# Performance work log

Hardware: AMD Instinct MI355X
Metric: run time of the kernel (lower is better)

## Reference

```python
import jax, jax.numpy as jnp
import numpy as np

B, S, D = 4, 4096, 1024

def setup_inputs() -> dict:
    key = jax.random.key(0)
    k1, k2 = jax.random.split(key)
    x = jax.random.normal(k1, (B, S, D), dtype=jnp.float32)
    W_qkv = jax.random.normal(k2, (D, 3 * D), dtype=jnp.float32) * (D ** -0.5)
    b_qkv = jnp.zeros((3 * D,), dtype=jnp.float32)
    return {"x": x, "W_qkv": W_qkv, "b_qkv": b_qkv}

def reference(x, W_qkv, b_qkv):
    # qkv projection: [B,S,3D]
    qkv = jnp.einsum('bsd,de->bse', x, W_qkv) + b_qkv
    q, k, v = jnp.split(qkv, 3, axis=-1)  # each [B,S,D]
    scale = q.shape[-1] ** -0.5
    # full [B,S,S] score matrix, as in the original (non-fused) implementation
    scores = jnp.einsum('bqd,bkd->bqk', q, k) * scale
    attn = jax.nn.softmax(scores, axis=-1)
    out = jnp.einsum('bqk,bkd->bqd', attn, v)
    return out
```

## Files before the change

### kernel.cpp

```cpp
#include <hip/hip_runtime.h>
#include <math.h>

typedef unsigned short ushort_t;
typedef __attribute__((ext_vector_type(8))) short short8;
typedef __attribute__((ext_vector_type(4))) float floatx4;

__device__ inline ushort_t f2bf(float x) {
    union { float f; unsigned int u; } c; c.f = x;
    unsigned int r = (c.u + 0x7fffu + ((c.u >> 16) & 1u)) >> 16;
    return (ushort_t)r;
}

__device__ __forceinline__ void glds16(const ushort_t* g, ushort_t* l) {
    __builtin_amdgcn_global_load_lds(
        (const __attribute__((address_space(1))) unsigned int*)g,
        (__attribute__((address_space(3))) unsigned int*)l,
        16, 0, 0);
}

__device__ __forceinline__ unsigned swzo(unsigned off) {
    return off ^ ((off >> 3) & 0x70u);
}

__global__ __launch_bounds__(256)
void wt_kernel(const float* __restrict__ W, ushort_t* __restrict__ Wt)
{
    __shared__ float tile[64][65];
    const int k0 = blockIdx.x * 64;
    const int n0 = blockIdx.y * 64;
    const int tid = threadIdx.x;
    #pragma unroll
    for (int ii = 0; ii < 16; ++ii) {
        int idx = ii * 256 + tid;
        int r = idx >> 6, c = idx & 63;
        tile[r][c] = W[(size_t)(k0 + r) * 3072 + n0 + c];
    }
    __syncthreads();
    #pragma unroll
    for (int ii = 0; ii < 16; ++ii) {
        int idx = ii * 256 + tid;
        int r = idx >> 6, c = idx & 63;
        Wt[(size_t)(n0 + r) * 1024 + k0 + c] = f2bf(tile[c][r]);
    }
}

__global__ __launch_bounds__(256)
void xcvt(const float* __restrict__ x, ushort_t* __restrict__ xb)
{
    const int i = (blockIdx.x * 256 + threadIdx.x) * 8;
    float4 f0 = *(const float4*)(x + i);
    float4 f1 = *(const float4*)(x + i + 4);
    ushort_t tmp[8] __attribute__((aligned(16)));
    tmp[0]=f2bf(f0.x); tmp[1]=f2bf(f0.y); tmp[2]=f2bf(f0.z); tmp[3]=f2bf(f0.w);
    tmp[4]=f2bf(f1.x); tmp[5]=f2bf(f1.y); tmp[6]=f2bf(f1.z); tmp[7]=f2bf(f1.w);
    *(uint4*)(xb + i) = *(const uint4*)tmp;
}

__global__ __launch_bounds__(256)
void qkv_mfma(const float* __restrict__ x, const ushort_t* __restrict__ Wt,
              const float* __restrict__ bias,
              ushort_t* __restrict__ q, ushort_t* __restrict__ k,
              ushort_t* __restrict__ vt)
{
    __shared__ ushort_t As[128][72];
    __shared__ ushort_t Bs[128][72];
    const int tid = threadIdx.x;
    const int w = tid >> 6, lane = tid & 63;
    const int m = lane & 15, quad = lane >> 4;
    const int col0 = blockIdx.x * 128;
    const int r0   = blockIdx.y * 128;

    floatx4 o[2][8];
    #pragma unroll
    for (int rf = 0; rf < 2; ++rf)
        #pragma unroll
        for (int nf = 0; nf < 8; ++nf)
            o[rf][nf] = (floatx4){0.f, 0.f, 0.f, 0.f};

    for (int kc = 0; kc < 16; ++kc) {
        const int kdim = kc * 64;
        __syncthreads();
        #pragma unroll
        for (int ii = 0; ii < 4; ++ii) {
            int lin = ii * 256 + tid;
            int row = lin >> 3, seg = lin & 7;
            const float* src = x + (size_t)(r0 + row) * 1024 + kdim + seg * 8;
            float4 f0 = *(const float4*)src;
            float4 f1 = *(const float4*)(src + 4);
            ushort_t tmp[8] __attribute__((aligned(16)));
            tmp[0]=f2bf(f0.x); tmp[1]=f2bf(f0.y); tmp[2]=f2bf(f0.z); tmp[3]=f2bf(f0.w);
            tmp[4]=f2bf(f1.x); tmp[5]=f2bf(f1.y); tmp[6]=f2bf(f1.z); tmp[7]=f2bf(f1.w);
            *(uint4*)&As[row][seg * 8] = *(const uint4*)tmp;
        }
        #pragma unroll
        for (int ii = 0; ii < 4; ++ii) {
            int lin = ii * 256 + tid;
            int row = lin >> 3, seg = lin & 7;
            const ushort_t* src = Wt + (size_t)(col0 + row) * 1024 + kdim + seg * 8;
            *(uint4*)&Bs[row][seg * 8] = *(const uint4*)src;
        }
        __syncthreads();
        #pragma unroll
        for (int kk = 0; kk < 2; ++kk) {
            short8 af[2];
            #pragma unroll
            for (int rf = 0; rf < 2; ++rf)
                af[rf] = *(const short8*)&As[w * 32 + rf * 16 + m][kk * 32 + quad * 8];
            #pragma unroll
            for (int nf = 0; nf < 8; ++nf) {
                short8 bf = *(const short8*)&Bs[nf * 16 + m][kk * 32 + quad * 8];
                #pragma unroll
                for (int rf = 0; rf < 2; ++rf)
                    o[rf][nf] = __builtin_amdgcn_mfma_f32_16x16x32_bf16(af[rf], bf, o[rf][nf], 0, 0, 0);
            }
        }
    }

    const int which = col0 >> 10;
    const int dbase = col0 & 1023;
    float bias_v[8];
    #pragma unroll
    for (int nf = 0; nf < 8; ++nf) bias_v[nf] = bias[col0 + nf * 16 + m];

    #pragma unroll
    for (int rf = 0; rf < 2; ++rf) {
        #pragma unroll
        for (int e = 0; e < 4; ++e) {
            const int g = r0 + w * 32 + rf * 16 + quad * 4 + e;
            #pragma unroll
            for (int nf = 0; nf < 8; ++nf) {
                const int c = dbase + nf * 16 + m;
                float val = o[rf][nf][e] + bias_v[nf];
                if (which == 0) {
                    q[(size_t)g * 1024 + c] = f2bf(val * 0.03125f);
                } else if (which == 1) {
                    k[(size_t)g * 1024 + c] = f2bf(val);
                } else {
                    vt[(size_t)(g >> 12) * 4194304 + (size_t)c * 4096 + (g & 4095)] = f2bf(val);
                }
            }
        }
    }
}

__global__ __launch_bounds__(256)
void qkv_mfma2(const ushort_t* __restrict__ xb, const ushort_t* __restrict__ Wt,
               const float* __restrict__ bias,
               ushort_t* __restrict__ q, ushort_t* __restrict__ k,
               ushort_t* __restrict__ vt)
{
    __shared__ __align__(1024) ushort_t As[128][64];
    __shared__ __align__(1024) ushort_t Bs[128][64];
    const int tid = threadIdx.x;
    const int w = tid >> 6, lane = tid & 63;
    const int m = lane & 15, quad = lane >> 4;
    const int lx = lane ^ ((lane >> 3) & 7);
    const int sr = lx >> 3, sc = (lx & 7) * 8;
    const int col0 = blockIdx.x * 128;
    const int r0   = blockIdx.y * 128;

    floatx4 o[2][8];
    #pragma unroll
    for (int rf = 0; rf < 2; ++rf)
        #pragma unroll
        for (int nf = 0; nf < 8; ++nf)
            o[rf][nf] = (floatx4){0.f, 0.f, 0.f, 0.f};

    for (int kc = 0; kc < 16; ++kc) {
        const int kdim = kc * 64;
        __syncthreads();
        #pragma unroll
        for (int ii = 0; ii < 4; ++ii) {
            glds16(xb + (size_t)(r0 + w * 32 + ii * 8 + sr) * 1024 + kdim + sc,
                   &As[w * 32 + ii * 8][0]);
            glds16(Wt + (size_t)(col0 + w * 32 + ii * 8 + sr) * 1024 + kdim + sc,
                   &Bs[w * 32 + ii * 8][0]);
        }
        __syncthreads();
        #pragma unroll
        for (int kk = 0; kk < 2; ++kk) {
            short8 af[2];
            #pragma unroll
            for (int rf = 0; rf < 2; ++rf)
                af[rf] = *(const short8*)((const char*)As +
                          swzo((unsigned)((w * 32 + rf * 16 + m) * 128 + kk * 64 + quad * 16)));
            #pragma unroll
            for (int nf = 0; nf < 8; ++nf) {
                short8 bf = *(const short8*)((const char*)Bs +
                          swzo((unsigned)((nf * 16 + m) * 128 + kk * 64 + quad * 16)));
                #pragma unroll
                for (int rf = 0; rf < 2; ++rf)
                    o[rf][nf] = __builtin_amdgcn_mfma_f32_16x16x32_bf16(af[rf], bf, o[rf][nf], 0, 0, 0);
            }
        }
    }

    const int which = col0 >> 10;
    const int dbase = col0 & 1023;
    float bias_v[8];
    #pragma unroll
    for (int nf = 0; nf < 8; ++nf) bias_v[nf] = bias[col0 + nf * 16 + m];

    #pragma unroll
    for (int rf = 0; rf < 2; ++rf) {
        #pragma unroll
        for (int e = 0; e < 4; ++e) {
            const int g = r0 + w * 32 + rf * 16 + quad * 4 + e;
            #pragma unroll
            for (int nf = 0; nf < 8; ++nf) {
                const int c = dbase + nf * 16 + m;
                float val = o[rf][nf][e] + bias_v[nf];
                if (which == 0) {
                    q[(size_t)g * 1024 + c] = f2bf(val * 0.03125f);
                } else if (which == 1) {
                    k[(size_t)g * 1024 + c] = f2bf(val);
                } else {
                    vt[(size_t)(g >> 12) * 4194304 + (size_t)c * 4096 + (g & 4095)] = f2bf(val);
                }
            }
        }
    }
}

__global__ __launch_bounds__(512, 2)
void fused_attn(const ushort_t* __restrict__ q, const ushort_t* __restrict__ kb_,
                const ushort_t* __restrict__ vt, float* __restrict__ out)
{
    __shared__ __align__(1024) unsigned char lds[135168];
    ushort_t (*Qs)[128][32] = (ushort_t(*)[128][32])(lds);
    ushort_t (*Ks)[256][32] = (ushort_t(*)[256][32])(lds + 16384);
    ushort_t (*Pls)[264]    = (ushort_t(*)[264])(lds);
    ushort_t (*Vs)[512][32] = (ushort_t(*)[512][32])(lds + 67584);
    float    (*redL)[4]     = (float(*)[4])(lds + 133120);

    const int tid  = threadIdx.x;
    const int w    = tid >> 6, lane = tid & 63;
    const int m    = lane & 15, quad = lane >> 4;
    const int wr   = w & 1, wc = w >> 1;
    const int lx   = lane ^ ((lane >> 3) & 7);
    const int lr   = lx >> 2, lc = (lx & 3) * 8;
    const int n0x  = blockIdx.x * 512;
    const int r0   = blockIdx.y * 128;
    const int b    = blockIdx.z;
    const size_t qoff = (size_t)b * 4096 * 1024;
    const size_t voff = (size_t)b * 4194304;

    unsigned qof[4], kof[4], vof[8];
    #pragma unroll
    for (int i = 0; i < 4; ++i)
        qof[i] = swzo((unsigned)((wr * 64 + i * 16 + m) * 64 + quad * 16));
    #pragma unroll
    for (int j = 0; j < 4; ++j)
        kof[j] = swzo((unsigned)((wc * 64 + j * 16 + m) * 64 + quad * 16));
    #pragma unroll
    for (int j = 0; j < 8; ++j)
        vof[j] = swzo((unsigned)((wc * 128 + j * 16 + m) * 64 + quad * 16));

    floatx4 o[4][8];
    #pragma unroll
    for (int i = 0; i < 4; ++i)
        #pragma unroll
        for (int j = 0; j < 8; ++j)
            o[i][j] = (floatx4){0.f, 0.f, 0.f, 0.f};
    float lsum[4][4] = {};

    for (int kt = 0; kt < 16; ++kt) {
        const int kbase = kt * 256;

        floatx4 s[4][4];
        #pragma unroll
        for (int i = 0; i < 4; ++i)
            #pragma unroll
            for (int j = 0; j < 4; ++j)
                s[i][j] = (floatx4){0.f, 0.f, 0.f, 0.f};

        {
            glds16(q   + qoff + (size_t)(r0 + w * 16 + lr) * 1024 + lc,             &Qs[0][w * 16][0]);
            glds16(kb_ + qoff + (size_t)(kbase + w * 32 + lr) * 1024 + lc,          &Ks[0][w * 32][0]);
            glds16(kb_ + qoff + (size_t)(kbase + w * 32 + 16 + lr) * 1024 + lc,     &Ks[0][w * 32 + 16][0]);
        }
        __syncthreads();
        for (int kc = 0; kc < 32; ++kc) {
            const int p = kc & 1;
            if (kc < 31) {
                const int kd = (kc + 1) * 32;
                glds16(q   + qoff + (size_t)(r0 + w * 16 + lr) * 1024 + kd + lc,         &Qs[p ^ 1][w * 16][0]);
                glds16(kb_ + qoff + (size_t)(kbase + w * 32 + lr) * 1024 + kd + lc,      &Ks[p ^ 1][w * 32][0]);
                glds16(kb_ + qoff + (size_t)(kbase + w * 32 + 16 + lr) * 1024 + kd + lc, &Ks[p ^ 1][w * 32 + 16][0]);
            }
            short8 af[4], bf[4];
            #pragma unroll
            for (int i = 0; i < 4; ++i)
                af[i] = *(const short8*)((const char*)Qs[p] + qof[i]);
            #pragma unroll
            for (int j = 0; j < 4; ++j)
                bf[j] = *(const short8*)((const char*)Ks[p] + kof[j]);
            #pragma unroll
            for (int i = 0; i < 4; ++i)
                #pragma unroll
                for (int j = 0; j < 4; ++j)
                    s[i][j] = __builtin_amdgcn_mfma_f32_16x16x32_bf16(af[i], bf[j], s[i][j], 0, 0, 0);
            __syncthreads();
        }

        #pragma unroll
        for (int i = 0; i < 4; ++i)
            #pragma unroll
            for (int j = 0; j < 4; ++j)
                #pragma unroll
                for (int e = 0; e < 4; ++e) {
                    float pv = __expf(s[i][j][e]);
                    lsum[i][e] += pv;
                    Pls[wr * 64 + i * 16 + quad * 4 + e][wc * 64 + j * 16 + m] = f2bf(pv);
                }

        {
            #pragma unroll
            for (int i = 0; i < 4; ++i)
                glds16(vt + voff + (size_t)(n0x + w * 64 + i * 16 + lr) * 4096 + kbase + lc,
                       &Vs[0][w * 64 + i * 16][0]);
        }
        __syncthreads();
        for (int vc = 0; vc < 8; ++vc) {
            const int p = vc & 1;
            if (vc < 7) {
                const int kd = kbase + (vc + 1) * 32;
                #pragma unroll
                for (int i = 0; i < 4; ++i)
                    glds16(vt + voff + (size_t)(n0x + w * 64 + i * 16 + lr) * 4096 + kd + lc,
                           &Vs[p ^ 1][w * 64 + i * 16][0]);
            }
            short8 ap[4], bv[8];
            #pragma unroll
            for (int i = 0; i < 4; ++i)
                ap[i] = *(const short8*)&Pls[wr * 64 + i * 16 + m][vc * 32 + quad * 8];
            #pragma unroll
            for (int j = 0; j < 8; ++j)
                bv[j] = *(const short8*)((const char*)Vs[p] + vof[j]);
            #pragma unroll
            for (int i = 0; i < 4; ++i)
                #pragma unroll
                for (int j = 0; j < 8; ++j)
                    o[i][j] = __builtin_amdgcn_mfma_f32_16x16x32_bf16(ap[i], bv[j], o[i][j], 0, 0, 0);
            __syncthreads();
        }
    }

    #pragma unroll
    for (int i = 0; i < 4; ++i)
        #pragma unroll
        for (int e = 0; e < 4; ++e) {
            float l = lsum[i][e];
            l += __shfl_xor(l, 1);
            l += __shfl_xor(l, 2);
            l += __shfl_xor(l, 4);
            l += __shfl_xor(l, 8);
            if (m == 0) redL[wr * 64 + i * 16 + quad * 4 + e][wc] = l;
        }
    __syncthreads();
    #pragma unroll
    for (int i = 0; i < 4; ++i)
        #pragma unroll
        for (int e = 0; e < 4; ++e) {
            const int row = wr * 64 + i * 16 + quad * 4 + e;
            const float inv = 1.0f / (redL[row][0] + redL[row][1] + redL[row][2] + redL[row][3]);
            const int g = b * 4096 + r0 + row;
            #pragma unroll
            for (int j = 0; j < 8; ++j)
                out[(size_t)g * 1024 + n0x + wc * 128 + j * 16 + m] = o[i][j][e] * inv;
        }
}

extern "C" void kernel_launch(void* const* d_in, const int* in_sizes, int n_in,
                              void* d_out, int out_size, void* d_ws, size_t ws_size,
                              hipStream_t stream)
{
    const float* x    = (const float*)d_in[0];
    const float* W    = (const float*)d_in[1];
    const float* bias = (const float*)d_in[2];
    float* out = (float*)d_out;

    const size_t SZQ  = (size_t)4 * 4096 * 1024 * 2;
    const size_t SZWT = (size_t)3072 * 1024 * 2;
    const size_t SZXB = (size_t)4 * 4096 * 1024 * 2;
    const size_t NEED  = 3 * SZQ + SZWT;
    const size_t NEED2 = NEED + SZXB;
    if (ws_size < NEED) return;

    ushort_t* q  = (ushort_t*)d_ws;
    ushort_t* k  = (ushort_t*)((char*)d_ws + SZQ);
    ushort_t* vt = (ushort_t*)((char*)d_ws + 2 * SZQ);
    ushort_t* Wt = (ushort_t*)((char*)d_ws + 3 * SZQ);
    ushort_t* xb = (ushort_t*)((char*)d_ws + NEED);

    wt_kernel <<<dim3(16, 48),   256, 0, stream>>>(W, Wt);
    if (ws_size >= NEED2) {
        xcvt      <<<dim3(8192),    256, 0, stream>>>(x, xb);
        qkv_mfma2 <<<dim3(24, 128), 256, 0, stream>>>(xb, Wt, bias, q, k, vt);
    } else {
        qkv_mfma  <<<dim3(24, 128), 256, 0, stream>>>(x, Wt, bias, q, k, vt);
    }
    fused_attn<<<dim3(2, 32, 4), 512, 0, stream>>>(q, k, vt, out);
}
```

Baseline: 795.8 us.

## Triple-buffer Q/K LDS loads with vmcnt waits and single barrier per step

Switches the QK^T inner loop from double to triple buffering of Q and K tiles in LDS. It replaces the trailing __syncthreads with an explicit vmcnt wait followed by a raw s_barrier, so loads for the next chunk overlap compute and one barrier per iteration is removed. It also raises wave priority around MFMA blocks in both the QK and PV loops. The change grows LDS usage and depends on a hand-placed waitcnt being correct for the global_load_lds ordering.

```diff
diff --git a/kernel.cpp b/kernel.cpp
--- a/kernel.cpp
+++ b/kernel.cpp
@@ -4,6 +4,8 @@
 typedef unsigned short ushort_t;
 typedef __attribute__((ext_vector_type(8))) short short8;
 typedef __attribute__((ext_vector_type(4))) float floatx4;
+
+#define VMCNT(n) asm volatile("s_waitcnt vmcnt(" #n ")" ::: "memory")
 
 __device__ inline ushort_t f2bf(float x) {
     union { float f; unsigned int u; } c; c.f = x;
@@ -226,12 +228,12 @@
 void fused_attn(const ushort_t* __restrict__ q, const ushort_t* __restrict__ kb_,
                 const ushort_t* __restrict__ vt, float* __restrict__ out)
 {
-    __shared__ __align__(1024) unsigned char lds[135168];
+    __shared__ __align__(1024) unsigned char lds[141312];
     ushort_t (*Qs)[128][32] = (ushort_t(*)[128][32])(lds);
-    ushort_t (*Ks)[256][32] = (ushort_t(*)[256][32])(lds + 16384);
+    ushort_t (*Ks)[256][32] = (ushort_t(*)[256][32])(lds + 24576);
     ushort_t (*Pls)[264]    = (ushort_t(*)[264])(lds);
-    ushort_t (*Vs)[512][32] = (ushort_t(*)[512][32])(lds + 67584);
-    float    (*redL)[4]     = (float(*)[4])(lds + 133120);
+    ushort_t (*Vs)[512][32] = (ushort_t(*)[512][32])(lds + 73728);
+    float    (*redL)[4]     = (float(*)[4])(lds + 139264);
 
     const int tid  = threadIdx.x;
     const int w    = tid >> 6, lane = tid & 63;
@@ -256,6 +258,10 @@
     for (int j = 0; j < 8; ++j)
         vof[j] = swzo((unsigned)((wc * 128 + j * 16 + m) * 64 + quad * 16));
 
+    const ushort_t* qsrc  = q   + qoff + (size_t)(r0 + w * 16 + lr) * 1024 + lc;
+    const ushort_t* ksrc0 = kb_ + qoff + (size_t)(w * 32 + lr) * 1024 + lc;
+    const ushort_t* ksrc1 = kb_ + qoff + (size_t)(w * 32 + 16 + lr) * 1024 + lc;
+
     floatx4 o[4][8];
     #pragma unroll
     for (int i = 0; i < 4; ++i)
@@ -274,34 +280,42 @@
             for (int j = 0; j < 4; ++j)
                 s[i][j] = (floatx4){0.f, 0.f, 0.f, 0.f};
 
+        glds16(qsrc,                        &Qs[0][w * 16][0]);
+        glds16(ksrc0 + (size_t)kbase * 1024, &Ks[0][w * 32][0]);
+        glds16(ksrc1 + (size_t)kbase * 1024, &Ks[0][w * 32 + 16][0]);
         {
-            glds16(q   + qoff + (size_t)(r0 + w * 16 + lr) * 1024 + lc,             &Qs[0][w * 16][0]);
-            glds16(kb_ + qoff + (size_t)(kbase + w * 32 + lr) * 1024 + lc,          &Ks[0][w * 32][0]);
-            glds16(kb_ + qoff + (size_t)(kbase + w * 32 + 16 + lr) * 1024 + lc,     &Ks[0][w * 32 + 16][0]);
-        }
-        __syncthreads();
-        for (int kc = 0; kc < 32; ++kc) {
-            const int p = kc & 1;
-            if (kc < 31) {
-                const int kd = (kc + 1) * 32;
-                glds16(q   + qoff + (size_t)(r0 + w * 16 + lr) * 1024 + kd + lc,         &Qs[p ^ 1][w * 16][0]);
-                glds16(kb_ + qoff + (size_t)(kbase + w * 32 + lr) * 1024 + kd + lc,      &Ks[p ^ 1][w * 32][0]);
-                glds16(kb_ + qoff + (size_t)(kbase + w * 32 + 16 + lr) * 1024 + kd + lc, &Ks[p ^ 1][w * 32 + 16][0]);
-            }
-            short8 af[4], bf[4];
-            #pragma unroll
-            for (int i = 0; i < 4; ++i)
-                af[i] = *(const short8*)((const char*)Qs[p] + qof[i]);
-            #pragma unroll
-            for (int j = 0; j < 4; ++j)
-                bf[j] = *(const short8*)((const char*)Ks[p] + kof[j]);
-            #pragma unroll
-            for (int i = 0; i < 4; ++i)
+            int cur = 0;
+            for (int kc = 0; kc < 32; ++kc) {
+                if (kc < 31) {
+                    const int nxt = (cur == 2) ? 0 : cur + 1;
+                    const int kd = (kc + 1) * 32;
+                    glds16(qsrc + kd,                             &Qs[nxt][w * 16][0]);
+                    glds16(ksrc0 + (size_t)kbase * 1024 + kd,     &Ks[nxt][w * 32][0]);
+                    glds16(ksrc1 + (size_t)kbase * 1024 + kd,     &Ks[nxt][w * 32 + 16][0]);
+                    VMCNT(3);
+                } else {
+                    VMCNT(0);
+                }
+                __builtin_amdgcn_s_barrier();
+                __builtin_amdgcn_sched_barrier(0);
+                short8 af[4], bf[4];
+                #pragma unroll
+                for (int i = 0; i < 4; ++i)
+                    af[i] = *(const short8*)((const char*)Qs[cur] + qof[i]);
                 #pragma unroll
                 for (int j = 0; j < 4; ++j)
-                    s[i][j] = __builtin_amdgcn_mfma_f32_16x16x32_bf16(af[i], bf[j], s[i][j], 0, 0, 0);
-            __syncthreads();
-        }
+                    bf[j] = *(const short8*)((const char*)Ks[cur] + kof[j]);
+                __builtin_amdgcn_s_setprio(1);
+                #pragma unroll
+                for (int i = 0; i < 4; ++i)
+                    #pragma unroll
+                    for (int j = 0; j < 4; ++j)
+                        s[i][j] = __builtin_amdgcn_mfma_f32_16x16x32_bf16(af[i], bf[j], s[i][j], 0, 0, 0);
+                __builtin_amdgcn_s_setprio(0);
+                cur = (cur == 2) ? 0 : cur + 1;
+            }
+        }
+        __syncthreads();
 
         #pragma unroll
         for (int i = 0; i < 4; ++i)
@@ -337,11 +351,13 @@
             #pragma unroll
             for (int j = 0; j < 8; ++j)
                 bv[j] = *(const short8*)((const char*)Vs[p] + vof[j]);
+            __builtin_amdgcn_s_setprio(1);
             #pragma unroll
             for (int i = 0; i < 4; ++i)
                 #pragma unroll
                 for (int j = 0; j < 8; ++j)
                     o[i][j] = __builtin_amdgcn_mfma_f32_16x16x32_bf16(ap[i], bv[j], o[i][j], 0, 0, 0);
+            __builtin_amdgcn_s_setprio(0);
             __syncthreads();
         }
     }
```

Result: faster. 756.2 us (-5.0%).
